# Performance work log

Hardware: AMD Instinct MI355X
Metric: run time of the kernel (lower is better)

Reference implementation:

```python
import jax, jax.numpy as jnp
import numpy as np

EMBED_DIM = 1024
NUM_HEADS = 16
HEAD_DIM = EMBED_DIM // NUM_HEADS
MLP_SIZE = 4096
LN_EPS = 1e-5


def setup_inputs() -> dict:
    key = jax.random.key(0)
    ks = jax.random.split(key, 12)
    d, f = EMBED_DIM, MLP_SIZE
    s = lambda fan_in: 1.0 / np.sqrt(fan_in)
    return {
        "x": jax.random.normal(ks[0], (2, 2048, d), dtype=jnp.float32),
        "ln1_g": jnp.ones((d,), jnp.float32),
        "ln1_b": jnp.zeros((d,), jnp.float32),
        "ln2_g": jnp.ones((d,), jnp.float32),
        "ln2_b": jnp.zeros((d,), jnp.float32),
        "w_qkv": jax.random.uniform(ks[1], (d, 3 * d), jnp.float32, -s(d), s(d)),
        "b_qkv": jax.random.uniform(ks[2], (3 * d,), jnp.float32, -s(d), s(d)),
        "w_proj": jax.random.uniform(ks[3], (d, d), jnp.float32, -s(d), s(d)),
        "b_proj": jax.random.uniform(ks[4], (d,), jnp.float32, -s(d), s(d)),
        "w_fc1": jax.random.uniform(ks[5], (d, f), jnp.float32, -s(d), s(d)),
        "b_fc1": jax.random.uniform(ks[6], (f,), jnp.float32, -s(d), s(d)),
        "w_fc2": jax.random.uniform(ks[7], (f, d), jnp.float32, -s(f), s(f)),
        "b_fc2": jax.random.uniform(ks[8], (d,), jnp.float32, -s(f), s(f)),
    }


def _layernorm(x, g, b):
    mu = jnp.mean(x, axis=-1, keepdims=True)
    var = jnp.mean(jnp.square(x - mu), axis=-1, keepdims=True)
    return (x - mu) * jax.lax.rsqrt(var + LN_EPS) * g + b


def reference(x, ln1_g, ln1_b, ln2_g, ln2_b, w_qkv, b_qkv, w_proj, b_proj,
              w_fc1, b_fc1, w_fc2, b_fc2):
    B, N, C = x.shape
    H, D = NUM_HEADS, HEAD_DIM
    scale = D ** -0.5

    # --- attention sub-block (pre-LN) ---
    h = _layernorm(x, ln1_g, ln1_b)
    qkv = h @ w_qkv + b_qkv                      # [B,N,3C]
    qkv = qkv.reshape(B, N, 3, H, D)
    q, k, v = (jnp.moveaxis(qkv, 2, 0)[i].transpose(0, 2, 1, 3) for i in range(3))  # each [B,H,N,D]
    attn = jnp.einsum("bhnd,bhmd->bhnm", q, k) * scale
    attn = jax.nn.softmax(attn, axis=-1)
    o = jnp.einsum("bhnm,bhmd->bhnd", attn, v)   # [B,H,N,D]
    o = o.transpose(0, 2, 1, 3).reshape(B, N, C)
    x = x + (o @ w_proj + b_proj)

    # --- MLP sub-block (pre-LN) ---
    h = _layernorm(x, ln2_g, ln2_b)
    h = jax.nn.gelu(h @ w_fc1 + b_fc1, approximate=False)
    x = x + (h @ w_fc2 + b_fc2)
    return x
```

## Files before the change

kernel.cpp:

```cpp
#include <hip/hip_runtime.h>
#include <hip/hip_bf16.h>

typedef __attribute__((ext_vector_type(8))) __bf16 bf16x8;
typedef __attribute__((ext_vector_type(4))) float f32x4;
typedef unsigned short u16;

__device__ __forceinline__ float bf2f(u16 u) {
    unsigned int i = ((unsigned int)u) << 16;
    return __builtin_bit_cast(float, i);
}
__device__ __forceinline__ u16 f2bf_u16(float f) {
    __hip_bfloat16 h = __float2bfloat16(f);
    return *(u16*)&h;
}
__device__ __forceinline__ float gelu_f(float v) {
    return 0.5f * v * (1.0f + erff(v * 0.70710678118654752440f));
}
__device__ __forceinline__ bool is_f32(const unsigned* p) { return *p == 0x3F800000u; }
__device__ __forceinline__ bf16x8 ld_bf8_b64x2(const u16* p) {
    uint2 lo = *(const uint2*)p;
    uint2 hi = *(const uint2*)(p + 4);
    uint4 v = make_uint4(lo.x, lo.y, hi.x, hi.y);
    return __builtin_bit_cast(bf16x8, v);
}
__device__ __forceinline__ void async16(const void* g, void* l) {
    __builtin_amdgcn_global_load_lds(
        (const __attribute__((address_space(1))) void*)g,
        (__attribute__((address_space(3))) void*)l, 16, 0, 0);
}

__device__ __forceinline__ void conv8(const void* src, u16* dst, long off, bool f32in) {
    if (f32in) {
        const float* s = (const float*)src + off;
        float4 a = *(const float4*)s, b = *(const float4*)(s + 4);
        u16 o[8] = {f2bf_u16(a.x), f2bf_u16(a.y), f2bf_u16(a.z), f2bf_u16(a.w),
                    f2bf_u16(b.x), f2bf_u16(b.y), f2bf_u16(b.z), f2bf_u16(b.w)};
        *(uint4*)(dst + off) = *(const uint4*)o;
    } else {
        *(uint4*)(dst + off) = *(const uint4*)((const u16*)src + off);
    }
}

__global__ __launch_bounds__(256) void conv_bias(
        const void* __restrict__ bq, const void* __restrict__ bp,
        const void* __restrict__ b1, const void* __restrict__ b2,
        u16* dbq, u16* dbp, u16* db1, u16* db2,
        const unsigned* __restrict__ dtp) {
    long e = ((long)blockIdx.x * 256 + threadIdx.x) * 8;
    if (e >= 9216L) return;
    bool f = is_f32(dtp);
    if      (e < 3072L) conv8(bq, dbq, e, f);
    else if (e < 4096L) conv8(bp, dbp, e - 3072L, f);
    else if (e < 8192L) conv8(b1, db1, e - 4096L, f);
    else                conv8(b2, db2, e - 8192L, f);
}

__global__ __launch_bounds__(256) void conv_t(const void* __restrict__ src,
                                              u16* __restrict__ dst,
                                              int K, int N,
                                              const unsigned* __restrict__ dtp) {
    const bool f32in = is_f32(dtp);
    __shared__ u16 T[64 * 68];
    int k0 = blockIdx.y * 64, n0 = blockIdx.x * 64;
    int t = threadIdx.x;
    int kr = t >> 2, nc = (t & 3) * 16;

    u16 tmp[16];
    if (f32in) {
        const float* s = (const float*)src + (size_t)(k0 + kr) * N + n0 + nc;
        float4 a = *(const float4*)s;
        float4 b = *(const float4*)(s + 4);
        float4 c = *(const float4*)(s + 8);
        float4 d = *(const float4*)(s + 12);
        tmp[0]=f2bf_u16(a.x);  tmp[1]=f2bf_u16(a.y);  tmp[2]=f2bf_u16(a.z);  tmp[3]=f2bf_u16(a.w);
        tmp[4]=f2bf_u16(b.x);  tmp[5]=f2bf_u16(b.y);  tmp[6]=f2bf_u16(b.z);  tmp[7]=f2bf_u16(b.w);
        tmp[8]=f2bf_u16(c.x);  tmp[9]=f2bf_u16(c.y);  tmp[10]=f2bf_u16(c.z); tmp[11]=f2bf_u16(c.w);
        tmp[12]=f2bf_u16(d.x); tmp[13]=f2bf_u16(d.y); tmp[14]=f2bf_u16(d.z); tmp[15]=f2bf_u16(d.w);
    } else {
        const u16* s = (const u16*)src + (size_t)(k0 + kr) * N + n0 + nc;
        *(uint4*)&tmp[0] = *(const uint4*)s;
        *(uint4*)&tmp[8] = *(const uint4*)(s + 8);
    }
    u16* dl = &T[kr * 68 + nc];
    #pragma unroll
    for (int j = 0; j < 4; ++j)
        *(uint2*)(dl + 4 * j) = *(const uint2*)&tmp[4 * j];
    __syncthreads();

    int nr = t >> 2, kc = (t & 3) * 16;
    u16 o[16];
    #pragma unroll
    for (int i = 0; i < 16; ++i) o[i] = T[(kc + i) * 68 + nr];
    u16* dp = dst + (size_t)(n0 + nr) * K + k0 + kc;
    *(uint4*)dp       = *(const uint4*)&o[0];
    *(uint4*)(dp + 8) = *(const uint4*)&o[8];
}

__global__ __launch_bounds__(256) void vt_prep(const u16* __restrict__ qkv,
                                               unsigned* __restrict__ vtg) {
    __shared__ unsigned Vt[64 * 32];
    int bx = blockIdx.x;
    int b = bx >> 9, h = (bx >> 5) & 15, kt = bx & 31;
    int t = threadIdx.x;
    int va = t & 31, vdc = t >> 5;
    size_t vb = ((size_t)(b * 2048 + kt * 64 + 2 * va)) * 3072 + 2048 + h * 64 + vdc * 8;
    uint4 v0 = *(const uint4*)(qkv + vb);
    uint4 v1 = *(const uint4*)(qkv + vb + 3072);
    const u16* p0 = (const u16*)&v0;
    const u16* p1 = (const u16*)&v1;
    #pragma unroll
    for (int j = 0; j < 8; ++j)
        Vt[(vdc * 8 + j) * 32 + va] = (unsigned)p0[j] | ((unsigned)p1[j] << 16);
    __syncthreads();
    unsigned* dst = vtg + (size_t)bx * 2048 + t * 8;
    *(uint4*)dst       = *(const uint4*)&Vt[t * 8];
    *(uint4*)(dst + 4) = *(const uint4*)&Vt[t * 8 + 4];
}

__global__ __launch_bounds__(256) void ln_first(const void* __restrict__ xin,
                                                const void* __restrict__ g,
                                                const void* __restrict__ b,
                                                __hip_bfloat16* __restrict__ out,
                                                const unsigned* __restrict__ dtp) {
    const bool f32in = is_f32(dtp);
    int row = blockIdx.x, t = threadIdx.x;
    size_t base = (size_t)row * 1024 + 4 * t;
    float v[4];
    if (f32in) {
        float4 f = *(const float4*)((const float*)xin + base);
        v[0] = f.x; v[1] = f.y; v[2] = f.z; v[3] = f.w;
    } else {
        ushort4 u = *(const ushort4*)((const __hip_bfloat16*)xin + base);
        v[0] = bf2f(u.x); v[1] = bf2f(u.y); v[2] = bf2f(u.z); v[3] = bf2f(u.w);
    }
    float s = v[0] + v[1] + v[2] + v[3];
    float s2 = v[0]*v[0] + v[1]*v[1] + v[2]*v[2] + v[3]*v[3];
    #pragma unroll
    for (int off = 32; off > 0; off >>= 1) {
        s  += __shfl_down(s, off);
        s2 += __shfl_down(s2, off);
    }
    __shared__ float red[8];
    int wave = t >> 6, lane = t & 63;
    if (lane == 0) { red[wave] = s; red[4 + wave] = s2; }
    __syncthreads();
    float S  = red[0] + red[1] + red[2] + red[3];
    float S2 = red[4] + red[5] + red[6] + red[7];
    float mean = S * (1.0f / 1024.0f);
    float var  = S2 * (1.0f / 1024.0f) - mean * mean;
    float rstd = rsqrtf(var + 1e-5f);
    float gg[4], bb[4];
    if (f32in) {
        float4 fg = *(const float4*)((const float*)g + 4 * t);
        float4 fb = *(const float4*)((const float*)b + 4 * t);
        gg[0]=fg.x; gg[1]=fg.y; gg[2]=fg.z; gg[3]=fg.w;
        bb[0]=fb.x; bb[1]=fb.y; bb[2]=fb.z; bb[3]=fb.w;
    } else {
        ushort4 ug = *(const ushort4*)((const __hip_bfloat16*)g + 4 * t);
        ushort4 ub = *(const ushort4*)((const __hip_bfloat16*)b + 4 * t);
        gg[0]=bf2f(ug.x); gg[1]=bf2f(ug.y); gg[2]=bf2f(ug.z); gg[3]=bf2f(ug.w);
        bb[0]=bf2f(ub.x); bb[1]=bf2f(ub.y); bb[2]=bf2f(ub.z); bb[3]=bf2f(ub.w);
    }
    #pragma unroll
    for (int i = 0; i < 4; ++i)
        out[base + i] = __float2bfloat16((v[i] - mean) * rstd * gg[i] + bb[i]);
}

__global__ __launch_bounds__(256) void ln_mid(const float* __restrict__ x,
                                              const void* __restrict__ g,
                                              const void* __restrict__ b,
                                              __hip_bfloat16* __restrict__ out,
                                              const unsigned* __restrict__ dtp) {
    const bool f32in = is_f32(dtp);
    int row = blockIdx.x, t = threadIdx.x;
    size_t base = (size_t)row * 1024 + 4 * t;
    float4 f = *(const float4*)(x + base);
    float v[4] = {f.x, f.y, f.z, f.w};
    float s = v[0] + v[1] + v[2] + v[3];
    float s2 = v[0]*v[0] + v[1]*v[1] + v[2]*v[2] + v[3]*v[3];
    #pragma unroll
    for (int off = 32; off > 0; off >>= 1) {
        s  += __shfl_down(s, off);
        s2 += __shfl_down(s2, off);
    }
    __shared__ float red[8];
    int wave = t >> 6, lane = t & 63;
    if (lane == 0) { red[wave] = s; red[4 + wave] = s2; }
    __syncthreads();
    float S  = red[0] + red[1] + red[2] + red[3];
    float S2 = red[4] + red[5] + red[6] + red[7];
    float mean = S * (1.0f / 1024.0f);
    float var  = S2 * (1.0f / 1024.0f) - mean * mean;
    float rstd = rsqrtf(var + 1e-5f);
    float gg[4], bb[4];
    if (f32in) {
        float4 fg = *(const float4*)((const float*)g + 4 * t);
        float4 fb = *(const float4*)((const float*)b + 4 * t);
        gg[0]=fg.x; gg[1]=fg.y; gg[2]=fg.z; gg[3]=fg.w;
        bb[0]=fb.x; bb[1]=fb.y; bb[2]=fb.z; bb[3]=fb.w;
    } else {
        ushort4 ug = *(const ushort4*)((const __hip_bfloat16*)g + 4 * t);
        ushort4 ub = *(const ushort4*)((const __hip_bfloat16*)b + 4 * t);
        gg[0]=bf2f(ug.x); gg[1]=bf2f(ug.y); gg[2]=bf2f(ug.z); gg[3]=bf2f(ug.w);
        bb[0]=bf2f(ub.x); bb[1]=bf2f(ub.y); bb[2]=bf2f(ub.z); bb[3]=bf2f(ub.w);
    }
    #pragma unroll
    for (int i = 0; i < 4; ++i)
        out[base + i] = __float2bfloat16((v[i] - mean) * rstd * gg[i] + bb[i]);
}

template<int EPI, int BM, int BN>
__global__ __launch_bounds__(256, 2)
void gemm_bf16(const u16* __restrict__ A,
               const u16* __restrict__ BT,
               const u16* __restrict__ bias,
               const void* __restrict__ res,
               void* __restrict__ outp,
               int M, int N, int K,
               const unsigned* __restrict__ dtp) {
    constexpr int NI = BM / 32, NJ = BN / 32;
    constexpr int ASZ = BM * 32, BSZ = BN * 32;
    const bool f32in = is_f32(dtp);
    __shared__ __align__(16) u16 As[2 * ASZ];
    __shared__ __align__(16) u16 Bs[2 * BSZ];
    (void)M;

    int t = threadIdx.x;
    int w = t >> 6, lane = t & 63;
    int quad = lane >> 4, lq = lane & 15;
    int bm = blockIdx.y * BM, bn = blockIdx.x * BN;
    int wm = (w & 1) * (16 * NI), wn = (w >> 1) * (16 * NJ);

    int sr = lane >> 2, sc = (lane & 3) * 8;
    u16* aldst = &As[w * (BM * 8) + lane * 8];
    const u16* ag = A + (size_t)(bm + w * (BM / 4) + sr) * K + sc;
    u16* bldst = &Bs[w * (BN * 8) + lane * 8];
    const u16* bg = BT + (size_t)(bn + w * (BN / 4) + sr) * K + sc;

    f32x4 acc[NI][NJ];
    #pragma unroll
    for (int i = 0; i < NI; ++i)
        #pragma unroll
        for (int j = 0; j < NJ; ++j)
            #pragma unroll
            for (int r = 0; r < 4; ++r) acc[i][j][r] = 0.0f;

    async16(ag, aldst);
    if constexpr (BM == 128) async16(ag + (size_t)16 * K, aldst + 512);
    async16(bg, bldst);
    if constexpr (BN == 128) async16(bg + (size_t)16 * K, bldst + 512);

    const int nIter = K >> 5;
    for (int k = 0; k < nIter; ++k) {
        __syncthreads();
        int cur = k & 1;
        if (k + 1 < nIter) {
            int nxt = cur ^ 1;
            const u16* agn = ag + (size_t)(k + 1) * 32;
            async16(agn, aldst + nxt * ASZ);
            if constexpr (BM == 128) async16(agn + (size_t)16 * K, aldst + nxt * ASZ + 512);
            const u16* bgn = bg + (size_t)(k + 1) * 32;
            async16(bgn, bldst + nxt * BSZ);
            if constexpr (BN == 128) async16(bgn + (size_t)16 * K, bldst + nxt * BSZ + 512);
        }

        const u16* Ac = &As[cur * ASZ];
        const u16* Bc = &Bs[cur * BSZ];
        bf16x8 af[NI], bfr[NJ];
        #pragma unroll
        for (int i = 0; i < NI; ++i)
            af[i] = *(const bf16x8*)&Ac[(wm + 16 * i + lq) * 32 + quad * 8];
        #pragma unroll
        for (int j = 0; j < NJ; ++j)
            bfr[j] = *(const bf16x8*)&Bc[(wn + 16 * j + lq) * 32 + quad * 8];
        #pragma unroll
        for (int i = 0; i < NI; ++i)
            #pragma unroll
            for (int j = 0; j < NJ; ++j)
                acc[i][j] = __builtin_amdgcn_mfma_f32_16x16x32_bf16(af[i], bfr[j], acc[i][j], 0, 0, 0);
    }

    #pragma unroll
    for (int i = 0; i < NI; ++i) {
        #pragma unroll
        for (int j = 0; j < NJ; ++j) {
            #pragma unroll
            for (int r = 0; r < 4; ++r) {
                int row = bm + wm + 16 * i + quad * 4 + r;
                int col = bn + wn + 16 * j + lq;
                size_t idx = (size_t)row * N + col;
                float v = acc[i][j][r] + bf2f(bias[col]);
                if constexpr (EPI == 0) {
                    ((__hip_bfloat16*)outp)[idx] = __float2bfloat16(v);
                } else if constexpr (EPI == 1) {
                    v += f32in ? ((const float*)res)[idx]
                               : bf2f(((const u16*)res)[idx]);
                    ((float*)outp)[idx] = v;
                } else if constexpr (EPI == 2) {
                    ((__hip_bfloat16*)outp)[idx] = __float2bfloat16(gelu_f(v));
                } else {
                    v += ((const float*)res)[idx];
                    if (f32in) ((float*)outp)[idx] = v;
                    else       ((__hip_bfloat16*)outp)[idx] = __float2bfloat16(v);
                }
            }
        }
    }
}

__global__ __launch_bounds__(256, 4)
void attn_mfma(const __hip_bfloat16* __restrict__ qkv,
               const unsigned* __restrict__ vtg,
               __hip_bfloat16* __restrict__ o_out) {
    __shared__ __align__(16) u16 Ks[64 * 72];
    __shared__ __align__(16) unsigned Vt[64 * 36];
    __shared__ __align__(16) u16 Ps[64 * 68];

    int t = threadIdx.x;
    int lane = t & 63, w = t >> 6;
    int quad = lane >> 4, lq = lane & 15;
    int bx = blockIdx.x;
    int b  = bx >> 9, h = (bx >> 5) & 15, qt = bx & 31;
    size_t tok0 = (size_t)b * 2048;

    {
        int key = t >> 2, ld = (t & 3) * 16;
        size_t qb = (tok0 + (size_t)qt * 64 + key) * 3072 + h * 64 + ld;
        uint4 a0 = *(const uint4*)(qkv + qb);
        uint4 a1 = *(const uint4*)(qkv + qb + 8);
        const u16* s0 = (const u16*)&a0;
        const u16* s1 = (const u16*)&a1;
        u16 q16[16];
        #pragma unroll
        for (int j = 0; j < 8; ++j) {
            q16[j]     = f2bf_u16(bf2f(s0[j]) * 0.125f);
            q16[8 + j] = f2bf_u16(bf2f(s1[j]) * 0.125f);
        }
        u16* dst = &Ps[key * 68 + ld];
        #pragma unroll
        for (int j4 = 0; j4 < 4; ++j4)
            *(uint2*)(dst + 4 * j4) = *(const uint2*)&q16[4 * j4];
    }
    __syncthreads();
    bf16x8 qf0 = ld_bf8_b64x2(&Ps[(w * 16 + lq) * 68 + quad * 8]);
    bf16x8 qf1 = ld_bf8_b64x2(&Ps[(w * 16 + lq) * 68 + quad * 8 + 32]);

    f32x4 oacc[4];
    #pragma unroll
    for (int dt = 0; dt < 4; ++dt)
        #pragma unroll
        for (int r = 0; r < 4; ++r) oacc[dt][r] = 0.0f;
    float m_run = -1e30f, l_run = 0.0f;

    int skey = t >> 2, sld = (t & 3) * 16;
    int vrow = t >> 2, vcol = (t & 3) * 8;

    uint4 k0, k1, w0, w1;
    {
        size_t kb = (tok0 + (size_t)skey) * 3072 + 1024 + h * 64 + sld;
        k0 = *(const uint4*)(qkv + kb);
        k1 = *(const uint4*)(qkv + kb + 8);
        const unsigned* vg = vtg + ((size_t)(b * 512 + h * 32)) * 2048 + t * 8;
        w0 = *(const uint4*)vg;
        w1 = *(const uint4*)(vg + 4);
    }

    for (int kt = 0; kt < 32; ++kt) {
        __syncthreads();
        *(uint4*)&Ks[skey * 72 + sld]     = k0;
        *(uint4*)&Ks[skey * 72 + sld + 8] = k1;
        unsigned* vdst = &Vt[vrow * 36 + vcol];
        *(uint4*)vdst       = w0;
        *(uint4*)(vdst + 4) = w1;
        __syncthreads();
        if (kt + 1 < 32) {
            size_t kb = (tok0 + (size_t)(kt + 1) * 64 + skey) * 3072 + 1024 + h * 64 + sld;
            k0 = *(const uint4*)(qkv + kb);
            k1 = *(const uint4*)(qkv + kb + 8);
            const unsigned* vg = vtg + ((size_t)(b * 512 + h * 32 + kt + 1)) * 2048 + t * 8;
            w0 = *(const uint4*)vg;
            w1 = *(const uint4*)(vg + 4);
        }

        f32x4 sacc[4];
        #pragma unroll
        for (int j = 0; j < 4; ++j)
            #pragma unroll
            for (int r = 0; r < 4; ++r) sacc[j][r] = 0.0f;
        #pragma unroll
        for (int j = 0; j < 4; ++j) {
            const u16* kr = &Ks[(j * 16 + lq) * 72 + quad * 8];
            bf16x8 kf0 = *(const bf16x8*)kr;
            bf16x8 kf1 = *(const bf16x8*)(kr + 32);
            sacc[j] = __builtin_amdgcn_mfma_f32_16x16x32_bf16(kf0, qf0, sacc[j], 0, 0, 0);
            sacc[j] = __builtin_amdgcn_mfma_f32_16x16x32_bf16(kf1, qf1, sacc[j], 0, 0, 0);
        }

        float mx = sacc[0][0];
        #pragma unroll
        for (int j = 0; j < 4; ++j)
            #pragma unroll
            for (int r = 0; r < 4; ++r) mx = fmaxf(mx, sacc[j][r]);
        mx = fmaxf(mx, __shfl_xor(mx, 16));
        mx = fmaxf(mx, __shfl_xor(mx, 32));
        if (!__all(mx <= m_run + 8.0f)) {
            float mnew = fmaxf(m_run, mx);
            float alpha = __expf(m_run - mnew);
            l_run *= alpha;
            #pragma unroll
            for (int dt = 0; dt < 4; ++dt)
                #pragma unroll
                for (int r = 0; r < 4; ++r) oacc[dt][r] *= alpha;
            m_run = mnew;
        }

        float ls = 0.0f;
        int prow = (w * 16 + lq) * 68;
        #pragma unroll
        for (int j = 0; j < 4; ++j) {
            float p0 = __expf(sacc[j][0] - m_run);
            float p1 = __expf(sacc[j][1] - m_run);
            float p2 = __expf(sacc[j][2] - m_run);
            float p3 = __expf(sacc[j][3] - m_run);
            ls += (p0 + p1) + (p2 + p3);
            u16 pk[4] = {f2bf_u16(p0), f2bf_u16(p1), f2bf_u16(p2), f2bf_u16(p3)};
            *(uint2*)&Ps[prow + quad * 4 + 16 * j] = *(const uint2*)pk;
        }
        ls += __shfl_xor(ls, 16);
        ls += __shfl_xor(ls, 32);
        l_run += ls;

        bf16x8 pf0 = ld_bf8_b64x2(&Ps[prow + quad * 8]);
        bf16x8 pf1 = ld_bf8_b64x2(&Ps[prow + quad * 8 + 32]);
        #pragma unroll
        for (int dt = 0; dt < 4; ++dt) {
            const unsigned* vr = &Vt[(dt * 16 + lq) * 36 + quad * 4];
            bf16x8 vf0 = __builtin_bit_cast(bf16x8, *(const uint4*)vr);
            bf16x8 vf1 = __builtin_bit_cast(bf16x8, *(const uint4*)(vr + 16));
            oacc[dt] = __builtin_amdgcn_mfma_f32_16x16x32_bf16(vf0, pf0, oacc[dt], 0, 0, 0);
            oacc[dt] = __builtin_amdgcn_mfma_f32_16x16x32_bf16(vf1, pf1, oacc[dt], 0, 0, 0);
        }
    }

    __syncthreads();
    u16* T = Ks;
    float inv = 1.0f / l_run;
    int trow = (w * 16 + lq) * 68;
    #pragma unroll
    for (int dt = 0; dt < 4; ++dt) {
        u16 pk[4] = {f2bf_u16(oacc[dt][0] * inv), f2bf_u16(oacc[dt][1] * inv),
                     f2bf_u16(oacc[dt][2] * inv), f2bf_u16(oacc[dt][3] * inv)};
        *(uint2*)&T[trow + quad * 4 + 16 * dt] = *(const uint2*)pk;
    }
    __syncthreads();
    {
        int q = t >> 2, dc = (t & 3) * 16;
        const u16* src = &T[q * 68 + dc];
        uint2 a0 = *(const uint2*)src;
        uint2 a1 = *(const uint2*)(src + 4);
        uint2 a2 = *(const uint2*)(src + 8);
        uint2 a3 = *(const uint2*)(src + 12);
        u16* op = (u16*)o_out + (tok0 + (size_t)qt * 64 + q) * 1024 + h * 64 + dc;
        *(uint4*)op       = make_uint4(a0.x, a0.y, a1.x, a1.y);
        *(uint4*)(op + 8) = make_uint4(a2.x, a2.y, a3.x, a3.y);
    }
}

extern "C" void kernel_launch(void* const* d_in, const int* in_sizes, int n_in,
                              void* d_out, int out_size, void* d_ws, size_t ws_size,
                              hipStream_t stream) {
    (void)in_sizes; (void)n_in; (void)out_size; (void)ws_size;
    const void* x      = d_in[0];
    const void* ln1_g  = d_in[1];
    const void* ln1_b  = d_in[2];
    const void* ln2_g  = d_in[3];
    const void* ln2_b  = d_in[4];
    const void* w_qkv  = d_in[5];
    const void* b_qkv  = d_in[6];
    const void* w_proj = d_in[7];
    const void* b_proj = d_in[8];
    const void* w_fc1  = d_in[9];
    const void* b_fc1  = d_in[10];
    const void* w_fc2  = d_in[11];
    const void* b_fc2  = d_in[12];
    const unsigned* probe = (const unsigned*)ln1_g;

    constexpr int Mtok = 4096;
    char* ws = (char*)d_ws;
    __hip_bfloat16* bufA = (__hip_bfloat16*)ws;
    __hip_bfloat16* qkvb = (__hip_bfloat16*)(ws + ((size_t)8 << 20));
    float*          x1   = (float*)(ws + ((size_t)8 << 20));
    u16*            w1T  = (u16*)(ws + ((size_t)24 << 20));
    u16*            wqT  = (u16*)(ws + ((size_t)32 << 20));
    u16*            wpT  = (u16*)(ws + ((size_t)38 << 20));
    unsigned*       vtg  = (unsigned*)(ws + ((size_t)40 << 20));
    __hip_bfloat16* g1   = (__hip_bfloat16*)(ws + ((size_t)32 << 20));
    u16*            w2T  = (u16*)ws;
    char* BZ = ws + ((size_t)64 << 20);
    u16* bqb = (u16*)BZ;
    u16* bpb = (u16*)(BZ + 8192);
    u16* b1b = (u16*)(BZ + 16384);
    u16* b2b = (u16*)(BZ + 24576);

    conv_bias<<<5, 256, 0, stream>>>(b_qkv, b_proj, b_fc1, b_fc2,
                                     bqb, bpb, b1b, b2b, probe);
    conv_t<<<dim3(3072 / 64, 1024 / 64), 256, 0, stream>>>(w_qkv, wqT, 1024, 3072, probe);
    conv_t<<<dim3(1024 / 64, 1024 / 64), 256, 0, stream>>>(w_proj, wpT, 1024, 1024, probe);
    ln_first<<<Mtok, 256, 0, stream>>>(x, ln1_g, ln1_b, bufA, probe);
    gemm_bf16<0, 128, 128><<<dim3(3072 / 128, Mtok / 128), 256, 0, stream>>>(
        (const u16*)bufA, wqT, bqb, nullptr, qkvb, Mtok, 3072, 1024, probe);
    vt_prep<<<1024, 256, 0, stream>>>((const u16*)qkvb, vtg);
    attn_mfma<<<1024, 256, 0, stream>>>(qkvb, vtg, bufA);
    conv_t<<<dim3(4096 / 64, 1024 / 64), 256, 0, stream>>>(w_fc1, w1T, 1024, 4096, probe);
    gemm_bf16<1, 128, 64><<<dim3(1024 / 64, Mtok / 128), 256, 0, stream>>>(
        (const u16*)bufA, wpT, bpb, x, x1, Mtok, 1024, 1024, probe);
    ln_mid<<<Mtok, 256, 0, stream>>>(x1, ln2_g, ln2_b, bufA, probe);
    gemm_bf16<2, 128, 128><<<dim3(4096 / 128, Mtok / 128), 256, 0, stream>>>(
        (const u16*)bufA, w1T, b1b, nullptr, g1, Mtok, 4096, 1024, probe);
    conv_t<<<dim3(1024 / 64, 4096 / 64), 256, 0, stream>>>(w_fc2, w2T, 4096, 1024, probe);
    gemm_bf16<3, 128, 64><<<dim3(1024 / 64, Mtok / 128), 256, 0, stream>>>(
        (const u16*)g1, w2T, b2b, x1, d_out, Mtok, 1024, 4096, probe);
}
```

Before: 400.2 us.

## Split-K FC2 GEMM with atomics, smaller proj tiles, MFMA priority in attention

The FC2 GEMM is split along K into two halves that atomically accumulate into a buffer pre-initialised with residual plus bias. A conversion pass follows for bf16 outputs. The projection GEMM moves to 64x64 tiles to launch more blocks. The attention kernel raises wave priority around its MFMA sections. The aim is better CU occupancy for the N=1024 GEMMs, at the cost of extra init/convert kernels and fp32 atomic traffic.

Result: slower. 410.0 us (+2.4%).

```diff
diff --git a/kernel.cpp b/kernel.cpp
--- a/kernel.cpp
+++ b/kernel.cpp
@@ -209,6 +209,30 @@
         out[base + i] = __float2bfloat16((v[i] - mean) * rstd * gg[i] + bb[i]);
 }
 
+__global__ __launch_bounds__(256) void fc2_init(float* __restrict__ x1,
+                                                const u16* __restrict__ b2,
+                                                float* __restrict__ dout,
+                                                const unsigned* __restrict__ dtp) {
+    const bool f32in = is_f32(dtp);
+    size_t i4 = ((size_t)blockIdx.x * 256 + threadIdx.x) * 4;
+    float4 v = *(const float4*)(x1 + i4);
+    int col = (int)(i4 & 1023);
+    ushort4 bb = *(const ushort4*)(b2 + col);
+    v.x += bf2f(bb.x); v.y += bf2f(bb.y); v.z += bf2f(bb.z); v.w += bf2f(bb.w);
+    float* o = f32in ? dout : x1;
+    *(float4*)(o + i4) = v;
+}
+
+__global__ __launch_bounds__(256) void fc2_cvt(const float* __restrict__ xacc,
+                                               u16* __restrict__ dout,
+                                               const unsigned* __restrict__ dtp) {
+    if (is_f32(dtp)) return;
+    size_t i4 = ((size_t)blockIdx.x * 256 + threadIdx.x) * 4;
+    float4 v = *(const float4*)(xacc + i4);
+    u16 o[4] = {f2bf_u16(v.x), f2bf_u16(v.y), f2bf_u16(v.z), f2bf_u16(v.w)};
+    *(uint2*)(dout + i4) = *(const uint2*)o;
+}
+
 template<int EPI, int BM, int BN>
 __global__ __launch_bounds__(256, 2)
 void gemm_bf16(const u16* __restrict__ A,
@@ -231,11 +255,14 @@
     int bm = blockIdx.y * BM, bn = blockIdx.x * BN;
     int wm = (w & 1) * (16 * NI), wn = (w >> 1) * (16 * NJ);
 
+    int Kl = K, k0 = 0;
+    if constexpr (EPI == 4) { Kl = K >> 1; k0 = blockIdx.z * Kl; }
+
     int sr = lane >> 2, sc = (lane & 3) * 8;
     u16* aldst = &As[w * (BM * 8) + lane * 8];
-    const u16* ag = A + (size_t)(bm + w * (BM / 4) + sr) * K + sc;
+    const u16* ag = A + (size_t)(bm + w * (BM / 4) + sr) * K + k0 + sc;
     u16* bldst = &Bs[w * (BN * 8) + lane * 8];
-    const u16* bg = BT + (size_t)(bn + w * (BN / 4) + sr) * K + sc;
+    const u16* bg = BT + (size_t)(bn + w * (BN / 4) + sr) * K + k0 + sc;
 
     f32x4 acc[NI][NJ];
     #pragma unroll
@@ -250,7 +277,7 @@
     async16(bg, bldst);
     if constexpr (BN == 128) async16(bg + (size_t)16 * K, bldst + 512);
 
-    const int nIter = K >> 5;
+    const int nIter = Kl >> 5;
     for (int k = 0; k < nIter; ++k) {
         __syncthreads();
         int cur = k & 1;
@@ -280,6 +307,8 @@
                 acc[i][j] = __builtin_amdgcn_mfma_f32_16x16x32_bf16(af[i], bfr[j], acc[i][j], 0, 0, 0);
     }
 
+    float* atgt = nullptr;
+    if constexpr (EPI == 4) atgt = f32in ? (float*)outp : (float*)res;
     #pragma unroll
     for (int i = 0; i < NI; ++i) {
         #pragma unroll
@@ -289,19 +318,19 @@
                 int row = bm + wm + 16 * i + quad * 4 + r;
                 int col = bn + wn + 16 * j + lq;
                 size_t idx = (size_t)row * N + col;
-                float v = acc[i][j][r] + bf2f(bias[col]);
-                if constexpr (EPI == 0) {
-                    ((__hip_bfloat16*)outp)[idx] = __float2bfloat16(v);
-                } else if constexpr (EPI == 1) {
-                    v += f32in ? ((const float*)res)[idx]
-                               : bf2f(((const u16*)res)[idx]);
-                    ((float*)outp)[idx] = v;
-                } else if constexpr (EPI == 2) {
-                    ((__hip_bfloat16*)outp)[idx] = __float2bfloat16(gelu_f(v));
+                if constexpr (EPI == 4) {
+                    atomicAdd(&atgt[idx], acc[i][j][r]);
                 } else {
-                    v += ((const float*)res)[idx];
-                    if (f32in) ((float*)outp)[idx] = v;
-                    else       ((__hip_bfloat16*)outp)[idx] = __float2bfloat16(v);
+                    float v = acc[i][j][r] + bf2f(bias[col]);
+                    if constexpr (EPI == 0) {
+                        ((__hip_bfloat16*)outp)[idx] = __float2bfloat16(v);
+                    } else if constexpr (EPI == 1) {
+                        v += f32in ? ((const float*)res)[idx]
+                                   : bf2f(((const u16*)res)[idx]);
+                        ((float*)outp)[idx] = v;
+                    } else if constexpr (EPI == 2) {
+                        ((__hip_bfloat16*)outp)[idx] = __float2bfloat16(gelu_f(v));
+                    }
                 }
             }
         }
@@ -387,6 +416,7 @@
         for (int j = 0; j < 4; ++j)
             #pragma unroll
             for (int r = 0; r < 4; ++r) sacc[j][r] = 0.0f;
+        __builtin_amdgcn_s_setprio(1);
         #pragma unroll
         for (int j = 0; j < 4; ++j) {
             const u16* kr = &Ks[(j * 16 + lq) * 72 + quad * 8];
@@ -395,6 +425,7 @@
             sacc[j] = __builtin_amdgcn_mfma_f32_16x16x32_bf16(kf0, qf0, sacc[j], 0, 0, 0);
             sacc[j] = __builtin_amdgcn_mfma_f32_16x16x32_bf16(kf1, qf1, sacc[j], 0, 0, 0);
         }
+        __builtin_amdgcn_s_setprio(0);
 
         float mx = sacc[0][0];
         #pragma unroll
@@ -432,6 +463,7 @@
 
         bf16x8 pf0 = ld_bf8_b64x2(&Ps[prow + quad * 8]);
         bf16x8 pf1 = ld_bf8_b64x2(&Ps[prow + quad * 8 + 32]);
+        __builtin_amdgcn_s_setprio(1);
         #pragma unroll
         for (int dt = 0; dt < 4; ++dt) {
             const unsigned* vr = &Vt[(dt * 16 + lq) * 36 + quad * 4];
@@ -440,6 +472,7 @@
             oacc[dt] = __builtin_amdgcn_mfma_f32_16x16x32_bf16(vf0, pf0, oacc[dt], 0, 0, 0);
             oacc[dt] = __builtin_amdgcn_mfma_f32_16x16x32_bf16(vf1, pf1, oacc[dt], 0, 0, 0);
         }
+        __builtin_amdgcn_s_setprio(0);
     }
 
     __syncthreads();
@@ -512,12 +545,14 @@
     vt_prep<<<1024, 256, 0, stream>>>((const u16*)qkvb, vtg);
     attn_mfma<<<1024, 256, 0, stream>>>(qkvb, vtg, bufA);
     conv_t<<<dim3(4096 / 64, 1024 / 64), 256, 0, stream>>>(w_fc1, w1T, 1024, 4096, probe);
-    gemm_bf16<1, 128, 64><<<dim3(1024 / 64, Mtok / 128), 256, 0, stream>>>(
+    gemm_bf16<1, 64, 64><<<dim3(1024 / 64, Mtok / 64), 256, 0, stream>>>(
         (const u16*)bufA, wpT, bpb, x, x1, Mtok, 1024, 1024, probe);
     ln_mid<<<Mtok, 256, 0, stream>>>(x1, ln2_g, ln2_b, bufA, probe);
     gemm_bf16<2, 128, 128><<<dim3(4096 / 128, Mtok / 128), 256, 0, stream>>>(
         (const u16*)bufA, w1T, b1b, nullptr, g1, Mtok, 4096, 1024, probe);
     conv_t<<<dim3(1024 / 64, 4096 / 64), 256, 0, stream>>>(w_fc2, w2T, 4096, 1024, probe);
-    gemm_bf16<3, 128, 64><<<dim3(1024 / 64, Mtok / 128), 256, 0, stream>>>(
+    fc2_init<<<4096, 256, 0, stream>>>(x1, b2b, (float*)d_out, probe);
+    gemm_bf16<4, 64, 64><<<dim3(1024 / 64, Mtok / 64, 2), 256, 0, stream>>>(
         (const u16*)g1, w2T, b2b, x1, d_out, Mtok, 1024, 4096, probe);
-}
+    fc2_cvt<<<4096, 256, 0, stream>>>(x1, (u16*)d_out, probe);
+}
```

## Add BK template with XOR-swizzled LDS, smaller tiles for N=1024 GEMMs, MFMA priority

Applied to the files above, without the earlier changes.

Makes the GEMM K-tile size a template parameter and XOR-swizzles the LDS column chunk by row, which targets bank conflicts on the fragment reads. The two N=1024 GEMMs (proj and fc2) switch to 64x64 tiles with BK=64, doubling grid size so more CUs are busy, at the cost of less reuse per tile. The attention kernel also wraps its MFMA sections in s_setprio so matrix work gets issue priority over other waves.

New measurement: 372.7 us. -6.9%, faster.

```diff
diff --git a/kernel.cpp b/kernel.cpp
--- a/kernel.cpp
+++ b/kernel.cpp
@@ -209,7 +209,7 @@
         out[base + i] = __float2bfloat16((v[i] - mean) * rstd * gg[i] + bb[i]);
 }
 
-template<int EPI, int BM, int BN>
+template<int EPI, int BM, int BN, int BK>
 __global__ __launch_bounds__(256, 2)
 void gemm_bf16(const u16* __restrict__ A,
                const u16* __restrict__ BT,
@@ -219,7 +219,12 @@
                int M, int N, int K,
                const unsigned* __restrict__ dtp) {
     constexpr int NI = BM / 32, NJ = BN / 32;
-    constexpr int ASZ = BM * 32, BSZ = BN * 32;
+    constexpr int ASZ = BM * BK, BSZ = BN * BK;
+    constexpr int SMASK = BK / 8 - 1;
+    constexpr int SBITS = (BK == 32) ? 2 : 3;
+    constexpr int RPA   = 512 / BK;
+    constexpr int NASYA = (BM * BK) / 2048;
+    constexpr int NASYB = (BN * BK) / 2048;
     const bool f32in = is_f32(dtp);
     __shared__ __align__(16) u16 As[2 * ASZ];
     __shared__ __align__(16) u16 Bs[2 * BSZ];
@@ -231,11 +236,12 @@
     int bm = blockIdx.y * BM, bn = blockIdx.x * BN;
     int wm = (w & 1) * (16 * NI), wn = (w >> 1) * (16 * NJ);
 
-    int sr = lane >> 2, sc = (lane & 3) * 8;
-    u16* aldst = &As[w * (BM * 8) + lane * 8];
-    const u16* ag = A + (size_t)(bm + w * (BM / 4) + sr) * K + sc;
-    u16* bldst = &Bs[w * (BN * 8) + lane * 8];
-    const u16* bg = BT + (size_t)(bn + w * (BN / 4) + sr) * K + sc;
+    int sr = lane >> SBITS;
+    int scs = ((lane & SMASK) ^ (sr & SMASK)) * 8;
+    u16* aldst = &As[w * (BM * BK / 4) + lane * 8];
+    const u16* ag = A + (size_t)(bm + w * (BM / 4) + sr) * K + scs;
+    u16* bldst = &Bs[w * (BN * BK / 4) + lane * 8];
+    const u16* bg = BT + (size_t)(bn + w * (BN / 4) + sr) * K + scs;
 
     f32x4 acc[NI][NJ];
     #pragma unroll
@@ -245,39 +251,50 @@
             #pragma unroll
             for (int r = 0; r < 4; ++r) acc[i][j][r] = 0.0f;
 
-    async16(ag, aldst);
-    if constexpr (BM == 128) async16(ag + (size_t)16 * K, aldst + 512);
-    async16(bg, bldst);
-    if constexpr (BN == 128) async16(bg + (size_t)16 * K, bldst + 512);
-
-    const int nIter = K >> 5;
+    #pragma unroll
+    for (int j = 0; j < NASYA; ++j)
+        async16(ag + (size_t)(j * RPA) * K, aldst + j * 512);
+    #pragma unroll
+    for (int j = 0; j < NASYB; ++j)
+        async16(bg + (size_t)(j * RPA) * K, bldst + j * 512);
+
+    const int nIter = K / BK;
     for (int k = 0; k < nIter; ++k) {
         __syncthreads();
         int cur = k & 1;
         if (k + 1 < nIter) {
             int nxt = cur ^ 1;
-            const u16* agn = ag + (size_t)(k + 1) * 32;
-            async16(agn, aldst + nxt * ASZ);
-            if constexpr (BM == 128) async16(agn + (size_t)16 * K, aldst + nxt * ASZ + 512);
-            const u16* bgn = bg + (size_t)(k + 1) * 32;
-            async16(bgn, bldst + nxt * BSZ);
-            if constexpr (BN == 128) async16(bgn + (size_t)16 * K, bldst + nxt * BSZ + 512);
+            const u16* agn = ag + (size_t)(k + 1) * BK;
+            #pragma unroll
+            for (int j = 0; j < NASYA; ++j)
+                async16(agn + (size_t)(j * RPA) * K, aldst + nxt * ASZ + j * 512);
+            const u16* bgn = bg + (size_t)(k + 1) * BK;
+            #pragma unroll
+            for (int j = 0; j < NASYB; ++j)
+                async16(bgn + (size_t)(j * RPA) * K, bldst + nxt * BSZ + j * 512);
         }
 
         const u16* Ac = &As[cur * ASZ];
         const u16* Bc = &Bs[cur * BSZ];
-        bf16x8 af[NI], bfr[NJ];
-        #pragma unroll
-        for (int i = 0; i < NI; ++i)
-            af[i] = *(const bf16x8*)&Ac[(wm + 16 * i + lq) * 32 + quad * 8];
-        #pragma unroll
-        for (int j = 0; j < NJ; ++j)
-            bfr[j] = *(const bf16x8*)&Bc[(wn + 16 * j + lq) * 32 + quad * 8];
-        #pragma unroll
-        for (int i = 0; i < NI; ++i)
-            #pragma unroll
-            for (int j = 0; j < NJ; ++j)
-                acc[i][j] = __builtin_amdgcn_mfma_f32_16x16x32_bf16(af[i], bfr[j], acc[i][j], 0, 0, 0);
+        #pragma unroll
+        for (int ks = 0; ks < BK / 32; ++ks) {
+            bf16x8 af[NI], bfr[NJ];
+            #pragma unroll
+            for (int i = 0; i < NI; ++i) {
+                int R = wm + 16 * i + lq;
+                af[i] = *(const bf16x8*)&Ac[R * BK + ((quad + ks * 4) ^ (R & SMASK)) * 8];
+            }
+            #pragma unroll
+            for (int j = 0; j < NJ; ++j) {
+                int R = wn + 16 * j + lq;
+                bfr[j] = *(const bf16x8*)&Bc[R * BK + ((quad + ks * 4) ^ (R & SMASK)) * 8];
+            }
+            #pragma unroll
+            for (int i = 0; i < NI; ++i)
+                #pragma unroll
+                for (int j = 0; j < NJ; ++j)
+                    acc[i][j] = __builtin_amdgcn_mfma_f32_16x16x32_bf16(af[i], bfr[j], acc[i][j], 0, 0, 0);
+        }
     }
 
     #pragma unroll
@@ -387,6 +404,7 @@
         for (int j = 0; j < 4; ++j)
             #pragma unroll
             for (int r = 0; r < 4; ++r) sacc[j][r] = 0.0f;
+        __builtin_amdgcn_s_setprio(1);
         #pragma unroll
         for (int j = 0; j < 4; ++j) {
             const u16* kr = &Ks[(j * 16 + lq) * 72 + quad * 8];
@@ -395,6 +413,7 @@
             sacc[j] = __builtin_amdgcn_mfma_f32_16x16x32_bf16(kf0, qf0, sacc[j], 0, 0, 0);
             sacc[j] = __builtin_amdgcn_mfma_f32_16x16x32_bf16(kf1, qf1, sacc[j], 0, 0, 0);
         }
+        __builtin_amdgcn_s_setprio(0);
 
         float mx = sacc[0][0];
         #pragma unroll
@@ -432,6 +451,7 @@
 
         bf16x8 pf0 = ld_bf8_b64x2(&Ps[prow + quad * 8]);
         bf16x8 pf1 = ld_bf8_b64x2(&Ps[prow + quad * 8 + 32]);
+        __builtin_amdgcn_s_setprio(1);
         #pragma unroll
         for (int dt = 0; dt < 4; ++dt) {
             const unsigned* vr = &Vt[(dt * 16 + lq) * 36 + quad * 4];
@@ -440,6 +460,7 @@
             oacc[dt] = __builtin_amdgcn_mfma_f32_16x16x32_bf16(vf0, pf0, oacc[dt], 0, 0, 0);
             oacc[dt] = __builtin_amdgcn_mfma_f32_16x16x32_bf16(vf1, pf1, oacc[dt], 0, 0, 0);
         }
+        __builtin_amdgcn_s_setprio(0);
     }
 
     __syncthreads();
@@ -507,17 +528,17 @@
     conv_t<<<dim3(3072 / 64, 1024 / 64), 256, 0, stream>>>(w_qkv, wqT, 1024, 3072, probe);
     conv_t<<<dim3(1024 / 64, 1024 / 64), 256, 0, stream>>>(w_proj, wpT, 1024, 1024, probe);
     ln_first<<<Mtok, 256, 0, stream>>>(x, ln1_g, ln1_b, bufA, probe);
-    gemm_bf16<0, 128, 128><<<dim3(3072 / 128, Mtok / 128), 256, 0, stream>>>(
+    gemm_bf16<0, 128, 128, 32><<<dim3(3072 / 128, Mtok / 128), 256, 0, stream>>>(
         (const u16*)bufA, wqT, bqb, nullptr, qkvb, Mtok, 3072, 1024, probe);
     vt_prep<<<1024, 256, 0, stream>>>((const u16*)qkvb, vtg);
     attn_mfma<<<1024, 256, 0, stream>>>(qkvb, vtg, bufA);
     conv_t<<<dim3(4096 / 64, 1024 / 64), 256, 0, stream>>>(w_fc1, w1T, 1024, 4096, probe);
-    gemm_bf16<1, 128, 64><<<dim3(1024 / 64, Mtok / 128), 256, 0, stream>>>(
+    gemm_bf16<1, 64, 64, 64><<<dim3(1024 / 64, Mtok / 64), 256, 0, stream>>>(
         (const u16*)bufA, wpT, bpb, x, x1, Mtok, 1024, 1024, probe);
     ln_mid<<<Mtok, 256, 0, stream>>>(x1, ln2_g, ln2_b, bufA, probe);
-    gemm_bf16<2, 128, 128><<<dim3(4096 / 128, Mtok / 128), 256, 0, stream>>>(
+    gemm_bf16<2, 128, 128, 32><<<dim3(4096 / 128, Mtok / 128), 256, 0, stream>>>(
         (const u16*)bufA, w1T, b1b, nullptr, g1, Mtok, 4096, 1024, probe);
     conv_t<<<dim3(1024 / 64, 4096 / 64), 256, 0, stream>>>(w_fc2, w2T, 4096, 1024, probe);
-    gemm_bf16<3, 128, 64><<<dim3(1024 / 64, Mtok / 128), 256, 0, stream>>>(
+    gemm_bf16<3, 64, 64, 64><<<dim3(1024 / 64, Mtok / 64), 256, 0, stream>>>(
         (const u16*)g1, w2T, b2b, x1, d_out, Mtok, 1024, 4096, probe);
 }
```
